# Kernel tuning notes

Measured on AMD Instinct MI355X. Metric: run time of the kernel, lower is better.

## Reference

```python
import jax, jax.numpy as jnp
import numpy as np

IN_FEATURES = 1024
OUT_FEATURES = 1024
NNZ = 104858  # round(0.1 * 1024 * 1024)
BATCH = 1024


def setup_inputs() -> dict:
    key = jax.random.key(0)
    k1, k2, k3, k4 = jax.random.split(key, 4)
    x = jax.random.normal(k1, (BATCH, IN_FEATURES), dtype=jnp.float32)
    weights = jax.random.normal(k2, (NNZ,), dtype=jnp.float32)
    bias = jax.random.normal(k3, (OUT_FEATURES,), dtype=jnp.float32)
    # COO indices: row in [0, OUT_FEATURES), col in [0, IN_FEATURES)
    indices = jax.random.randint(k4, (2, NNZ), 0, 1024, dtype=jnp.int64)
    return {"x": x, "weights": weights, "bias": bias, "indices": indices}


def reference(x, weights, bias, indices):
    # y[n, r] = sum_{k: row_k == r} w_k * x[n, col_k]  (unstructured COO spmm)
    row, col = indices[0], indices[1]
    # gather input columns per nnz entry: [nnz, N]
    gathered = x.T[col] * weights[:, None]
    # scatter-add into output rows: [out_features, N]
    out = jax.ops.segment_sum(gathered, row, num_segments=OUT_FEATURES)
    return out.T + bias  # [N, out_features]
```

## Files before the change

kernel.cpp:

```cpp
#include <hip/hip_runtime.h>
#include <hip/hip_bf16.h>

#define NNZ   104858
#define NB    1024
#define NIN   1024
#define NOUT  1024

typedef __bf16 bf16;
typedef bf16  bf16x8 __attribute__((ext_vector_type(8)));
typedef float f32x4  __attribute__((ext_vector_type(4)));

__global__ __launch_bounds__(256)
void k_pre(const float* __restrict__ x, float* __restrict__ Wd,
           bf16* __restrict__ xb) {
    const int b = blockIdx.x, t = threadIdx.x;
    if (b < 512) {
        float4 z = {0.f, 0.f, 0.f, 0.f};
        float4* w4 = (float4*)Wd;
        int i = (b * 256 + t) * 2;
        w4[i] = z; w4[i + 1] = z;
    } else {
        const int base = ((b - 512) * 256 + t) * 8;
        const float4* s4 = (const float4*)(x + base);
        float4 v0 = s4[0], v1 = s4[1];
        bf16x8 o;
        o[0] = (bf16)v0.x; o[1] = (bf16)v0.y; o[2] = (bf16)v0.z; o[3] = (bf16)v0.w;
        o[4] = (bf16)v1.x; o[5] = (bf16)v1.y; o[6] = (bf16)v1.z; o[7] = (bf16)v1.w;
        *(bf16x8*)(xb + base) = o;
    }
}

__global__ __launch_bounds__(256)
void k_densify(const int* __restrict__ idx, const float* __restrict__ w,
               float* __restrict__ Wd) {
    int k = blockIdx.x * 256 + threadIdx.x;
    if (k < NNZ) {
        int r = idx[k] & (NOUT - 1);
        int c = idx[NNZ + k] & (NIN - 1);
        atomicAdd(&Wd[r * NIN + c], w[k]);
    }
}

__device__ __forceinline__ void gload_lds16(const void* g, void* l) {
    __builtin_amdgcn_global_load_lds((const __attribute__((address_space(1))) void*)g,
                                     (__attribute__((address_space(3))) void*)l,
                                     16, 0, 0);
}

__global__ __launch_bounds__(512)
void k_gemm(const bf16* __restrict__ A, const float* __restrict__ Wd,
            const float* __restrict__ bias, float* __restrict__ out) {
    __shared__ __align__(16) bf16 As[2][64 * 64];
    __shared__ __align__(16) bf16 Bs[2][64 * 64];
    __shared__ f32x4 red[4][64][4];

    const int b  = blockIdx.x;
    const int id = (b & 7) * 32 + (b >> 3);
    const int m0 = (id & 15) * 64, n0 = (id >> 4) * 64;

    const int t    = threadIdx.x;
    const int lane = t & 63;
    const int wv   = t >> 6;
    const int half = wv >> 2;
    const int w4   = wv & 3, wr = w4 >> 1, wc = w4 & 1;
    const int fr   = lane & 15, fg = lane >> 4;

    const int th   = t & 255;
    const int srow = th >> 3;
    const int sg   = th & 7;
    const int brow = th >> 2;
    const int bq   = th & 3;

    f32x4 acc[2][2] = {};

    const float* wrow = Wd + (size_t)(n0 + brow) * NIN + half * 512;
    float4 bv0, bv1, bv2, bv3;
    {
        const float4* p = (const float4*)(wrow + bq * 16);
        bv0 = p[0]; bv1 = p[1]; bv2 = p[2]; bv3 = p[3];
    }

    for (int ks = 0; ks < 8; ++ks) {
        const int kbase = half * 512 + ks * 64;
        #pragma unroll
        for (int i = 0; i < 2; ++i) {
            int row = i * 32 + srow;
            int g2  = sg ^ (row & 7);
            gload_lds16(A + (size_t)(m0 + row) * NIN + kbase + g2 * 8,
                        As[half] + row * 64 + sg * 8);
        }
        {
            bf16x8 o0, o1;
            o0[0] = (bf16)bv0.x; o0[1] = (bf16)bv0.y; o0[2] = (bf16)bv0.z; o0[3] = (bf16)bv0.w;
            o0[4] = (bf16)bv1.x; o0[5] = (bf16)bv1.y; o0[6] = (bf16)bv1.z; o0[7] = (bf16)bv1.w;
            o1[0] = (bf16)bv2.x; o1[1] = (bf16)bv2.y; o1[2] = (bf16)bv2.z; o1[3] = (bf16)bv2.w;
            o1[4] = (bf16)bv3.x; o1[5] = (bf16)bv3.y; o1[6] = (bf16)bv3.z; o1[7] = (bf16)bv3.w;
            int g0 = (bq * 2)     ^ (brow & 7);
            int g1 = (bq * 2 + 1) ^ (brow & 7);
            *(bf16x8*)(Bs[half] + brow * 64 + g0 * 8) = o0;
            *(bf16x8*)(Bs[half] + brow * 64 + g1 * 8) = o1;
        }
        __syncthreads();

        if (ks < 7) {
            const float4* p = (const float4*)(wrow + (ks + 1) * 64 + bq * 16);
            bv0 = p[0]; bv1 = p[1]; bv2 = p[2]; bv3 = p[3];
        }

        bf16x8 af[2][2], bfr[2][2];
        #pragma unroll
        for (int mi = 0; mi < 2; ++mi) {
            int row = wr * 32 + mi * 16 + fr;
            #pragma unroll
            for (int kk = 0; kk < 2; ++kk) {
                int gsw = (kk * 4 + fg) ^ (row & 7);
                af[mi][kk] = *(const bf16x8*)(As[half] + row * 64 + gsw * 8);
            }
        }
        #pragma unroll
        for (int ni = 0; ni < 2; ++ni) {
            int row = wc * 32 + ni * 16 + fr;
            #pragma unroll
            for (int kk = 0; kk < 2; ++kk) {
                int gsw = (kk * 4 + fg) ^ (row & 7);
                bfr[ni][kk] = *(const bf16x8*)(Bs[half] + row * 64 + gsw * 8);
            }
        }
        #pragma unroll
        for (int mi = 0; mi < 2; ++mi)
            #pragma unroll
            for (int ni = 0; ni < 2; ++ni)
                #pragma unroll
                for (int kk = 0; kk < 2; ++kk)
                    acc[mi][ni] = __builtin_amdgcn_mfma_f32_16x16x32_bf16(
                        af[mi][kk], bfr[ni][kk], acc[mi][ni], 0, 0, 0);
        __syncthreads();
    }

    if (half == 1) {
        #pragma unroll
        for (int mi = 0; mi < 2; ++mi)
            #pragma unroll
            for (int ni = 0; ni < 2; ++ni)
                red[w4][lane][mi * 2 + ni] = acc[mi][ni];
    }
    __syncthreads();
    if (half == 0) {
        #pragma unroll
        for (int mi = 0; mi < 2; ++mi) {
            #pragma unroll
            for (int ni = 0; ni < 2; ++ni) {
                f32x4 p = red[w4][lane][mi * 2 + ni];
                int row0 = m0 + wr * 32 + mi * 16 + fg * 4;
                int col  = n0 + wc * 32 + ni * 16 + fr;
                float bb = bias[col];
                #pragma unroll
                for (int j = 0; j < 4; ++j)
                    out[(size_t)(row0 + j) * NOUT + col] = acc[mi][ni][j] + p[j] + bb;
            }
        }
    }
}

static inline size_t align256(size_t v) { return (v + 255) & ~(size_t)255; }

extern "C" void kernel_launch(void* const* d_in, const int* in_sizes, int n_in,
                              void* d_out, int out_size, void* d_ws, size_t ws_size,
                              hipStream_t stream) {
    const float* x    = (const float*)d_in[0];
    const float* wts  = (const float*)d_in[1];
    const float* bias = (const float*)d_in[2];
    const int*   idx  = (const int*)d_in[3];

    char* ws = (char*)d_ws;
    size_t off = 0;
    float* Wd = (float*)(ws + off); off = align256(off + (size_t)NOUT * NIN * 4);
    bf16*  xb = (bf16*) (ws + off); off = align256(off + (size_t)NB * NIN * 2);

    const int nb_nnz = (NNZ + 255) / 256;

    k_pre<<<1024, 256, 0, stream>>>(x, Wd, xb);
    k_densify<<<nb_nnz, 256, 0, stream>>>(idx, wts, Wd);
    k_gemm<<<256, 512, 0, stream>>>(xb, Wd, bias, (float*)d_out);
}
```

Measured before the change: 29.02 us.

## Fuse prep, densify and GEMM into one cooperative kernel with grid syncs

Merges the three launches (zero/convert, atomic densify, bf16 MFMA GEMM) into a single cooperative kernel of 256 blocks × 512 threads, using grid-wide syncs between the phases. This removes two kernel launch boundaries and their gaps. In exchange, each phase now runs on only 256 blocks, and grid.sync adds its own barrier cost. The densify step now covers 131072 threads, so all NNZ entries are still handled.

Measured after the change: 93.14 us. +220.9%, slower.

```diff
diff --git a/kernel.cpp b/kernel.cpp
--- a/kernel.cpp
+++ b/kernel.cpp
@@ -1,5 +1,8 @@
 #include <hip/hip_runtime.h>
 #include <hip/hip_bf16.h>
+#include <hip/hip_cooperative_groups.h>
+
+namespace cg = cooperative_groups;
 
 #define NNZ   104858
 #define NB    1024
@@ -10,17 +13,31 @@
 typedef bf16  bf16x8 __attribute__((ext_vector_type(8)));
 typedef float f32x4  __attribute__((ext_vector_type(4)));
 
-__global__ __launch_bounds__(256)
-void k_pre(const float* __restrict__ x, float* __restrict__ Wd,
-           bf16* __restrict__ xb) {
-    const int b = blockIdx.x, t = threadIdx.x;
-    if (b < 512) {
+__device__ __forceinline__ void gload_lds16(const void* g, void* l) {
+    __builtin_amdgcn_global_load_lds((const __attribute__((address_space(1))) void*)g,
+                                     (__attribute__((address_space(3))) void*)l,
+                                     16, 0, 0);
+}
+
+__global__ __launch_bounds__(512)
+void k_fused(const float* __restrict__ x, const float* __restrict__ wts,
+             const float* __restrict__ bias, const int* __restrict__ idx,
+             float* __restrict__ Wd, bf16* __restrict__ xb,
+             float* __restrict__ out) {
+    __shared__ __align__(16) bf16 As[2][64 * 64];
+    __shared__ __align__(16) bf16 Bs[2][64 * 64];
+    __shared__ f32x4 red[4][64][4];
+
+    cg::grid_group grid = cg::this_grid();
+    const int gid = blockIdx.x * 512 + threadIdx.x;
+
+    {
         float4 z = {0.f, 0.f, 0.f, 0.f};
         float4* w4 = (float4*)Wd;
-        int i = (b * 256 + t) * 2;
-        w4[i] = z; w4[i + 1] = z;
-    } else {
-        const int base = ((b - 512) * 256 + t) * 8;
+        w4[gid * 2]     = z;
+        w4[gid * 2 + 1] = z;
+
+        const int base = gid * 8;
         const float4* s4 = (const float4*)(x + base);
         float4 v0 = s4[0], v1 = s4[1];
         bf16x8 o;
@@ -28,31 +45,14 @@
         o[4] = (bf16)v1.x; o[5] = (bf16)v1.y; o[6] = (bf16)v1.z; o[7] = (bf16)v1.w;
         *(bf16x8*)(xb + base) = o;
     }
-}
+    grid.sync();
 
-__global__ __launch_bounds__(256)
-void k_densify(const int* __restrict__ idx, const float* __restrict__ w,
-               float* __restrict__ Wd) {
-    int k = blockIdx.x * 256 + threadIdx.x;
-    if (k < NNZ) {
-        int r = idx[k] & (NOUT - 1);
-        int c = idx[NNZ + k] & (NIN - 1);
-        atomicAdd(&Wd[r * NIN + c], w[k]);
+    if (gid < NNZ) {
+        int r = idx[gid] & (NOUT - 1);
+        int c = idx[NNZ + gid] & (NIN - 1);
+        atomicAdd(&Wd[r * NIN + c], wts[gid]);
     }
-}
-
-__device__ __forceinline__ void gload_lds16(const void* g, void* l) {
-    __builtin_amdgcn_global_load_lds((const __attribute__((address_space(1))) void*)g,
-                                     (__attribute__((address_space(3))) void*)l,
-                                     16, 0, 0);
-}
-
-__global__ __launch_bounds__(512)
-void k_gemm(const bf16* __restrict__ A, const float* __restrict__ Wd,
-            const float* __restrict__ bias, float* __restrict__ out) {
-    __shared__ __align__(16) bf16 As[2][64 * 64];
-    __shared__ __align__(16) bf16 Bs[2][64 * 64];
-    __shared__ f32x4 red[4][64][4];
+    grid.sync();
 
     const int b  = blockIdx.x;
     const int id = (b & 7) * 32 + (b >> 3);
@@ -62,7 +62,7 @@
     const int lane = t & 63;
     const int wv   = t >> 6;
     const int half = wv >> 2;
-    const int w4   = wv & 3, wr = w4 >> 1, wc = w4 & 1;
+    const int w4i  = wv & 3, wr = w4i >> 1, wc = w4i & 1;
     const int fr   = lane & 15, fg = lane >> 4;
 
     const int th   = t & 255;
@@ -86,7 +86,7 @@
         for (int i = 0; i < 2; ++i) {
             int row = i * 32 + srow;
             int g2  = sg ^ (row & 7);
-            gload_lds16(A + (size_t)(m0 + row) * NIN + kbase + g2 * 8,
+            gload_lds16(xb + (size_t)(m0 + row) * NIN + kbase + g2 * 8,
                         As[half] + row * 64 + sg * 8);
         }
         {
@@ -142,7 +142,7 @@
         for (int mi = 0; mi < 2; ++mi)
             #pragma unroll
             for (int ni = 0; ni < 2; ++ni)
-                red[w4][lane][mi * 2 + ni] = acc[mi][ni];
+                red[w4i][lane][mi * 2 + ni] = acc[mi][ni];
     }
     __syncthreads();
     if (half == 0) {
@@ -150,7 +150,7 @@
         for (int mi = 0; mi < 2; ++mi) {
             #pragma unroll
             for (int ni = 0; ni < 2; ++ni) {
-                f32x4 p = red[w4][lane][mi * 2 + ni];
+                f32x4 p = red[w4i][lane][mi * 2 + ni];
                 int row0 = m0 + wr * 32 + mi * 16 + fg * 4;
                 int col  = n0 + wc * 32 + ni * 16 + fr;
                 float bb = bias[col];
@@ -176,10 +176,10 @@
     size_t off = 0;
     float* Wd = (float*)(ws + off); off = align256(off + (size_t)NOUT * NIN * 4);
     bf16*  xb = (bf16*) (ws + off); off = align256(off + (size_t)NB * NIN * 2);
+    float* outp = (float*)d_out;
 
-    const int nb_nnz = (NNZ + 255) / 256;
-
-    k_pre<<<1024, 256, 0, stream>>>(x, Wd, xb);
-    k_densify<<<nb_nnz, 256, 0, stream>>>(idx, wts, Wd);
-    k_gemm<<<256, 512, 0, stream>>>(xb, Wd, bias, (float*)d_out);
+    void* args[] = {(void*)&x, (void*)&wts, (void*)&bias, (void*)&idx,
+                    (void*)&Wd, (void*)&xb, (void*)&outp};
+    hipLaunchCooperativeKernel((const void*)k_fused, dim3(256), dim3(512),
+                               args, 0, stream);
 }
```

## Double-buffer GEMM LDS tiles to overlap next-tile loads with MFMA

Applied to the files above, without the earlier changes.

The GEMM's A and B shared-memory tiles become double-buffered. The next K-slice's async global-to-LDS copy of A and the global load of B are issued before the current slice's MFMAs, and B's bf16 conversion and store go into the other buffer afterwards. This removes one barrier per iteration and hides load latency behind compute, at the cost of twice the LDS per block (64KB plus the reduction buffer), which may reduce occupancy.

Result: slower. 29.71 us (+2.4%).

```diff
diff --git a/kernel.cpp b/kernel.cpp
--- a/kernel.cpp
+++ b/kernel.cpp
@@ -50,8 +50,8 @@
 __global__ __launch_bounds__(512)
 void k_gemm(const bf16* __restrict__ A, const float* __restrict__ Wd,
             const float* __restrict__ bias, float* __restrict__ out) {
-    __shared__ __align__(16) bf16 As[2][64 * 64];
-    __shared__ __align__(16) bf16 Bs[2][64 * 64];
+    __shared__ __align__(16) bf16 As[2][2][64 * 64];
+    __shared__ __align__(16) bf16 Bs[2][2][64 * 64];
     __shared__ f32x4 red[4][64][4];
 
     const int b  = blockIdx.x;
@@ -62,7 +62,7 @@
     const int lane = t & 63;
     const int wv   = t >> 6;
     const int half = wv >> 2;
-    const int w4   = wv & 3, wr = w4 >> 1, wc = w4 & 1;
+    const int w4i  = wv & 3, wr = w4i >> 1, wc = w4i & 1;
     const int fr   = lane & 15, fg = lane >> 4;
 
     const int th   = t & 255;
@@ -74,37 +74,44 @@
     f32x4 acc[2][2] = {};
 
     const float* wrow = Wd + (size_t)(n0 + brow) * NIN + half * 512;
-    float4 bv0, bv1, bv2, bv3;
+
     {
-        const float4* p = (const float4*)(wrow + bq * 16);
-        bv0 = p[0]; bv1 = p[1]; bv2 = p[2]; bv3 = p[3];
-    }
-
-    for (int ks = 0; ks < 8; ++ks) {
-        const int kbase = half * 512 + ks * 64;
         #pragma unroll
         for (int i = 0; i < 2; ++i) {
             int row = i * 32 + srow;
             int g2  = sg ^ (row & 7);
-            gload_lds16(A + (size_t)(m0 + row) * NIN + kbase + g2 * 8,
-                        As[half] + row * 64 + sg * 8);
-        }
-        {
-            bf16x8 o0, o1;
-            o0[0] = (bf16)bv0.x; o0[1] = (bf16)bv0.y; o0[2] = (bf16)bv0.z; o0[3] = (bf16)bv0.w;
-            o0[4] = (bf16)bv1.x; o0[5] = (bf16)bv1.y; o0[6] = (bf16)bv1.z; o0[7] = (bf16)bv1.w;
-            o1[0] = (bf16)bv2.x; o1[1] = (bf16)bv2.y; o1[2] = (bf16)bv2.z; o1[3] = (bf16)bv2.w;
-            o1[4] = (bf16)bv3.x; o1[5] = (bf16)bv3.y; o1[6] = (bf16)bv3.z; o1[7] = (bf16)bv3.w;
-            int g0 = (bq * 2)     ^ (brow & 7);
-            int g1 = (bq * 2 + 1) ^ (brow & 7);
-            *(bf16x8*)(Bs[half] + brow * 64 + g0 * 8) = o0;
-            *(bf16x8*)(Bs[half] + brow * 64 + g1 * 8) = o1;
-        }
-        __syncthreads();
-
+            gload_lds16(A + (size_t)(m0 + row) * NIN + half * 512 + g2 * 8,
+                        As[half][0] + row * 64 + sg * 8);
+        }
+        const float4* p = (const float4*)(wrow + bq * 16);
+        float4 v0 = p[0], v1 = p[1], v2 = p[2], v3 = p[3];
+        bf16x8 o0, o1;
+        o0[0] = (bf16)v0.x; o0[1] = (bf16)v0.y; o0[2] = (bf16)v0.z; o0[3] = (bf16)v0.w;
+        o0[4] = (bf16)v1.x; o0[5] = (bf16)v1.y; o0[6] = (bf16)v1.z; o0[7] = (bf16)v1.w;
+        o1[0] = (bf16)v2.x; o1[1] = (bf16)v2.y; o1[2] = (bf16)v2.z; o1[3] = (bf16)v2.w;
+        o1[4] = (bf16)v3.x; o1[5] = (bf16)v3.y; o1[6] = (bf16)v3.z; o1[7] = (bf16)v3.w;
+        int g0 = (bq * 2)     ^ (brow & 7);
+        int g1 = (bq * 2 + 1) ^ (brow & 7);
+        *(bf16x8*)(Bs[half][0] + brow * 64 + g0 * 8) = o0;
+        *(bf16x8*)(Bs[half][0] + brow * 64 + g1 * 8) = o1;
+    }
+    __syncthreads();
+
+    for (int ks = 0; ks < 8; ++ks) {
+        const int cur = ks & 1, nxt = cur ^ 1;
+
+        float4 nv0, nv1, nv2, nv3;
         if (ks < 7) {
+            const int kb = half * 512 + (ks + 1) * 64;
+            #pragma unroll
+            for (int i = 0; i < 2; ++i) {
+                int row = i * 32 + srow;
+                int g2  = sg ^ (row & 7);
+                gload_lds16(A + (size_t)(m0 + row) * NIN + kb + g2 * 8,
+                            As[half][nxt] + row * 64 + sg * 8);
+            }
             const float4* p = (const float4*)(wrow + (ks + 1) * 64 + bq * 16);
-            bv0 = p[0]; bv1 = p[1]; bv2 = p[2]; bv3 = p[3];
+            nv0 = p[0]; nv1 = p[1]; nv2 = p[2]; nv3 = p[3];
         }
 
         bf16x8 af[2][2], bfr[2][2];
@@ -114,7 +121,7 @@
             #pragma unroll
             for (int kk = 0; kk < 2; ++kk) {
                 int gsw = (kk * 4 + fg) ^ (row & 7);
-                af[mi][kk] = *(const bf16x8*)(As[half] + row * 64 + gsw * 8);
+                af[mi][kk] = *(const bf16x8*)(As[half][cur] + row * 64 + gsw * 8);
             }
         }
         #pragma unroll
@@ -123,7 +130,7 @@
             #pragma unroll
             for (int kk = 0; kk < 2; ++kk) {
                 int gsw = (kk * 4 + fg) ^ (row & 7);
-                bfr[ni][kk] = *(const bf16x8*)(Bs[half] + row * 64 + gsw * 8);
+                bfr[ni][kk] = *(const bf16x8*)(Bs[half][cur] + row * 64 + gsw * 8);
             }
         }
         #pragma unroll
@@ -134,6 +141,18 @@
                 for (int kk = 0; kk < 2; ++kk)
                     acc[mi][ni] = __builtin_amdgcn_mfma_f32_16x16x32_bf16(
                         af[mi][kk], bfr[ni][kk], acc[mi][ni], 0, 0, 0);
+
+        if (ks < 7) {
+            bf16x8 o0, o1;
+            o0[0] = (bf16)nv0.x; o0[1] = (bf16)nv0.y; o0[2] = (bf16)nv0.z; o0[3] = (bf16)nv0.w;
+            o0[4] = (bf16)nv1.x; o0[5] = (bf16)nv1.y; o0[6] = (bf16)nv1.z; o0[7] = (bf16)nv1.w;
+            o1[0] = (bf16)nv2.x; o1[1] = (bf16)nv2.y; o1[2] = (bf16)nv2.z; o1[3] = (bf16)nv2.w;
+            o1[4] = (bf16)nv3.x; o1[5] = (bf16)nv3.y; o1[6] = (bf16)nv3.z; o1[7] = (bf16)nv3.w;
+            int g0 = (bq * 2)     ^ (brow & 7);
+            int g1 = (bq * 2 + 1) ^ (brow & 7);
+            *(bf16x8*)(Bs[half][nxt] + brow * 64 + g0 * 8) = o0;
+            *(bf16x8*)(Bs[half][nxt] + brow * 64 + g1 * 8) = o1;
+        }
         __syncthreads();
     }
 
@@ -142,7 +161,7 @@
         for (int mi = 0; mi < 2; ++mi)
             #pragma unroll
             for (int ni = 0; ni < 2; ++ni)
-                red[w4][lane][mi * 2 + ni] = acc[mi][ni];
+                red[w4i][lane][mi * 2 + ni] = acc[mi][ni];
     }
     __syncthreads();
     if (half == 0) {
@@ -150,7 +169,7 @@
         for (int mi = 0; mi < 2; ++mi) {
             #pragma unroll
             for (int ni = 0; ni < 2; ++ni) {
-                f32x4 p = red[w4][lane][mi * 2 + ni];
+                f32x4 p = red[w4i][lane][mi * 2 + ni];
                 int row0 = m0 + wr * 32 + mi * 16 + fg * 4;
                 int col  = n0 + wc * 32 + ni * 16 + fr;
                 float bb = bias[col];
```
